# Kernel optimization log

Hardware: AMD Instinct MI355X
Metric: run time of the kernel (lower is better)

Reference implementation:

```python
import jax, jax.numpy as jnp
import numpy as np
from jax import lax

EPS = 1e-5  # flax BatchNorm default epsilon

def _conv(x, k, b):
    y = lax.conv_general_dilated(x, k, (1, 1), 'SAME', dimension_numbers=('NHWC', 'HWIO', 'NHWC'))
    return y + b

def _bn(x, s, o, m, v):
    # BatchNorm with use_running_average=True (eval mode)
    return (x - m) * (s / jnp.sqrt(v + EPS)) + o

def _pool(x):
    return lax.reduce_window(x, -jnp.inf, lax.max, (1, 2, 2, 1), (1, 2, 2, 1), 'SAME')

def _lstm_last(x_seq, Wi, Wh, b):
    # x_seq: [T,B,D]; Wi: [L,D,4H]; Wh: [L,H,4H]; b: [L,4H].
    # Faithful to original bug: every layer consumes the SAME raw input x_seq
    # (layers are not stacked); only the last layer's hidden states are used.
    B = x_seq.shape[1]
    H = Wh.shape[1]
    def run_layer(Wi_l, Wh_l, b_l):
        def step(carry, xt):
            h, c = carry
            z = xt @ Wi_l + h @ Wh_l + b_l  # [B,4H]
            i, f, g, o = jnp.split(z, 4, axis=-1)
            c2 = jax.nn.sigmoid(f) * c + jax.nn.sigmoid(i) * jnp.tanh(g)
            h2 = jax.nn.sigmoid(o) * jnp.tanh(c2)
            return (h2, c2), h2
        init = (jnp.zeros((B, H), x_seq.dtype), jnp.zeros((B, H), x_seq.dtype))
        _, hs = lax.scan(step, init, x_seq)
        return hs  # [T,B,H]
    hs_all = jax.vmap(run_layer)(Wi, Wh, b)  # [L,T,B,H]
    return hs_all[-1]


def setup_inputs():
    key = jax.random.key(0)
    ks = iter(jax.random.split(key, 64))
    def nrm(shape, scale=0.05):
        return jax.random.normal(next(ks), shape, jnp.float32) * scale
    d = {}
    d['x'] = jax.random.normal(next(ks), (64, 32, 256, 1), jnp.float32)
    cin = [1, 64, 128, 256, 256]
    cout = [64, 128, 256, 256, 512]
    for i in range(5):
        d[f'k{i+1}'] = nrm((3, 3, cin[i], cout[i]))
        d[f'b{i+1}'] = nrm((cout[i],))
        d[f's{i+1}'] = 1.0 + nrm((cout[i],), 0.1)
        d[f'o{i+1}'] = nrm((cout[i],), 0.1)
        d[f'm{i+1}'] = jnp.zeros((cout[i],), jnp.float32)
        d[f'v{i+1}'] = jnp.ones((cout[i],), jnp.float32)
    L, D, H = 2, 2048, 512
    for pre in ('fw', 'bw'):
        d[f'{pre}_Wi'] = nrm((L, D, 4 * H), 0.02)
        d[f'{pre}_Wh'] = nrm((L, H, 4 * H), 0.02)
        d[f'{pre}_b'] = nrm((L, 4 * H), 0.02)
    d['fc_W'] = nrm((2 * H, 80), 0.02)
    d['fc_b'] = nrm((80,), 0.02)
    return d


def reference(x, k1, b1, k2, b2, k3, b3, k4, b4, k5, b5,
              s1, o1, m1, v1, s2, o2, m2, v2, s3, o3, m3, v3,
              s4, o4, m4, v4, s5, o5, m5, v5,
              fw_Wi, fw_Wh, fw_b, bw_Wi, bw_Wh, bw_b, fc_W, fc_b):
    # CNN stem (eval mode: dropout is identity, BN uses running stats)
    x = _pool(_bn(jax.nn.relu(_conv(x, k1, b1)), s1, o1, m1, v1))
    x = _pool(_bn(jax.nn.relu(_conv(x, k2, b2)), s2, o2, m2, v2))
    x = _pool(_bn(jax.nn.relu(_conv(x, k3, b3)), s3, o3, m3, v3))
    x = _bn(jax.nn.relu(_conv(x, k4, b4)), s4, o4, m4, v4)
    x = _bn(jax.nn.relu(_conv(x, k5, b5)), s5, o5, m5, v5)
    b, h, w, c = x.shape
    x = x.reshape(b, w, h * c)        # faithful raw reshape (no transpose), as in original
    x_seq = jnp.swapaxes(x, 0, 1)     # [T,B,D]
    fw = _lstm_last(x_seq, fw_Wi, fw_Wh, fw_b)          # [T,B,H]
    bw = _lstm_last(x_seq[::-1], bw_Wi, bw_Wh, bw_b)    # [T,B,H]; NOT re-flipped (matches original)
    out = jnp.swapaxes(jnp.concatenate([fw, bw], axis=-1), 0, 1)  # [B,T,2H]
    logits = out @ fc_W + fc_b
    return jax.nn.log_softmax(logits, axis=-1)
```

## Files before the change

### kernel.cpp

```cpp
#include <hip/hip_runtime.h>
#include <hip/hip_bf16.h>
#include <math.h>

#define EPSBN 1e-5f

using short8 = __attribute__((ext_vector_type(8))) short;
using f32x4  = __attribute__((ext_vector_type(4))) float;
using us4    = __attribute__((ext_vector_type(4))) unsigned short;

#define MFMA16(a, b, c) __builtin_amdgcn_mfma_f32_16x16x32_bf16(a, b, c, 0, 0, 0)

__device__ __forceinline__ float bf2f(unsigned short u) {
  unsigned int v = ((unsigned int)u) << 16;
  float f;
  __builtin_memcpy(&f, &v, 4);
  return f;
}
__device__ __forceinline__ unsigned short f2bf(float f) {
  __hip_bfloat16 h = __float2bfloat16(f);
  unsigned short u;
  __builtin_memcpy(&u, &h, 2);
  return u;
}
__device__ __forceinline__ float fast_sigmoid(float z) {
  return __builtin_amdgcn_rcpf(1.f + __expf(-z));
}
__device__ __forceinline__ float fast_tanh(float z) {
  float x2 = fminf(fmaxf(2.f * z, -30.f), 30.f);
  float e = __expf(x2);
  return (e - 1.f) * __builtin_amdgcn_rcpf(e + 1.f);
}
__device__ __forceinline__ void stage16(const unsigned short* g, unsigned short* l) {
  __builtin_amdgcn_global_load_lds(
      (const __attribute__((address_space(1))) void*)g,
      (__attribute__((address_space(3))) void*)l, 16, 0, 0);
}

__global__ __launch_bounds__(256) void conv1_pool(
    const float* __restrict__ in, const float* __restrict__ w,
    const float* __restrict__ bias, const float* __restrict__ sc,
    const float* __restrict__ of, const float* __restrict__ mn,
    const float* __restrict__ vr, unsigned short* __restrict__ out) {
  __shared__ float lds[4][258];
  __shared__ unsigned short obuf[128 * 64];
  const int blk = blockIdx.x;
  const int b = blk >> 4, y0 = blk & 15;
  const int tid = threadIdx.x;
  for (int i = tid; i < 4 * 258; i += 256) {
    int row = i / 258, c = i - row * 258;
    int iy = 2 * y0 - 1 + row, xx = c - 1;
    float v = 0.f;
    if ((unsigned)iy < 32u && (unsigned)xx < 256u)
      v = in[((b << 5) + iy) * 256 + xx];
    lds[row][c] = v;
  }
  __syncthreads();
  const int co = tid & 63, xg = tid >> 6;
  float w9[9];
  #pragma unroll
  for (int t = 0; t < 9; ++t) w9[t] = w[t * 64 + co];
  const float scale = sc[co] * rsqrtf(vr[co] + EPSBN);
  const float shift = of[co] - mn[co] * scale;
  const float bs = bias[co];
  for (int px = 0; px < 32; ++px) {
    const int xp = xg * 32 + px;
    float m = -1e30f;
    #pragma unroll
    for (int dy = 0; dy < 2; ++dy) {
      #pragma unroll
      for (int dx = 0; dx < 2; ++dx) {
        const int x = 2 * xp + dx;
        float acc = bs;
        #pragma unroll
        for (int r = 0; r < 3; ++r)
          #pragma unroll
          for (int cc = 0; cc < 3; ++cc)
            acc = fmaf(lds[dy + r][x + cc], w9[r * 3 + cc], acc);
        float v = fmaxf(acc, 0.f) * scale + shift;
        m = fmaxf(m, v);
      }
    }
    obuf[xp * 64 + co] = f2bf(m);
  }
  __syncthreads();
  unsigned short* orow = out + (((long)(b * 18 + y0 + 1) * 130 + 1) << 6);
  for (int i = tid; i < 1024; i += 256)
    *(short8*)(orow + i * 8) = *(const short8*)(obuf + i * 8);
}

template<int C, int H2, int W2>
__global__ __launch_bounds__(256) void maxpool_pad_vec(
    const unsigned short* __restrict__ in, unsigned short* __restrict__ out) {
  constexpr int W2P = W2 + 2, H2P = H2 + 2, C8 = C / 8;
  const long total = (long)64 * H2P * W2P * C8;
  long i = (long)blockIdx.x * 256 + threadIdx.x;
  if (i >= total) return;
  const int c8 = (int)(i % C8);
  long r = i / C8;
  const int xp = (int)(r % W2P); r /= W2P;
  const int yp = (int)(r % H2P);
  const int b = (int)(r / H2P);
  short8 res = {};
  if (yp >= 1 && yp <= H2 && xp >= 1 && xp <= W2) {
    const long rs = (long)(2 * W2) * C;
    const unsigned short* p0 =
        in + (((long)b * (2 * H2) + (yp - 1) * 2) * (2 * W2) + (xp - 1) * 2) * C + c8 * 8;
    short8 v00 = *(const short8*)(p0);
    short8 v01 = *(const short8*)(p0 + C);
    short8 v10 = *(const short8*)(p0 + rs);
    short8 v11 = *(const short8*)(p0 + rs + C);
    #pragma unroll
    for (int e = 0; e < 8; ++e) {
      float f0 = bf2f((unsigned short)v00[e]), f1 = bf2f((unsigned short)v01[e]);
      float f2 = bf2f((unsigned short)v10[e]), f3 = bf2f((unsigned short)v11[e]);
      float mx = fmaxf(fmaxf(f0, f1), fmaxf(f2, f3));
      unsigned short uu;
      if (mx == f0) uu = (unsigned short)v00[e];
      else if (mx == f1) uu = (unsigned short)v01[e];
      else if (mx == f2) uu = (unsigned short)v10[e];
      else uu = (unsigned short)v11[e];
      res[e] = (short)uu;
    }
  }
  *(short8*)(out + (((long)b * H2P + yp) * W2P + xp) * C + c8 * 8) = res;
}

struct TAll {
  const float* src[9];
  unsigned short* dst[9];
  int K[9];
  int N[9];
};
__global__ __launch_bounds__(256) void transpose_multi(TAll P) {
  const int z = blockIdx.z;
  const int K = P.K[z], N = P.N[z];
  const int k0 = blockIdx.x * 32, n0 = blockIdx.y * 32;
  if (k0 >= K || n0 >= N) return;
  __shared__ float T[32][33];
  const float* in = P.src[z];
  unsigned short* out = P.dst[z];
  const int tid = threadIdx.x;
  const int r = tid >> 3, c4 = (tid & 7) * 4;
  if (n0 + 32 <= N) {
    float4 v = *(const float4*)(in + (long)(k0 + r) * N + n0 + c4);
    T[r][c4 + 0] = v.x; T[r][c4 + 1] = v.y; T[r][c4 + 2] = v.z; T[r][c4 + 3] = v.w;
  } else {
    #pragma unroll
    for (int i = 0; i < 4; ++i) {
      int col = n0 + c4 + i;
      T[r][c4 + i] = (col < N) ? in[(long)(k0 + r) * N + col] : 0.f;
    }
  }
  __syncthreads();
  if (n0 + r < N) {
    us4 o;
    #pragma unroll
    for (int i = 0; i < 4; ++i) o[i] = f2bf(T[c4 + i][r]);
    *(us4*)(out + (long)(n0 + r) * K + k0 + c4) = o;
  }
}

__global__ __launch_bounds__(256) void zero_multi(
    float* p0, long n0, float* p1, long n1, float* p2, long n2, float* p3, long n3) {
  const long i0 = (long)blockIdx.x * 256 + threadIdx.x;
  const long st = (long)gridDim.x * 256;
  for (long j = i0; j < n0; j += st) p0[j] = 0.f;
  for (long j = i0; j < n1; j += st) p1[j] = 0.f;
  for (long j = i0; j < n2; j += st) p2[j] = 0.f;
  for (long j = i0; j < n3; j += st) p3[j] = 0.f;
}

template<int CIN, int COUT, int H, int W, int OUTPAD, int NBM, int NBN>
__global__ __launch_bounds__(256) void conv_mfma128(
    const unsigned short* __restrict__ act, const unsigned short* __restrict__ wT,
    const float* __restrict__ bias, const float* __restrict__ sc,
    const float* __restrict__ of, const float* __restrict__ mn,
    const float* __restrict__ vr, unsigned short* __restrict__ out) {
  constexpr int K9 = 9 * CIN;
  constexpr int HW = H * W;
  constexpr int WP = W + 2;
  constexpr int NK = K9 / 32;
  constexpr int NWG = NBM * NBN;
  constexpr int CSH = (CIN == 64) ? 1 : (CIN == 128) ? 2 : 3;
  constexpr int CMSK = (1 << CSH) - 1;
  __shared__ unsigned short As[2][4096];
  __shared__ unsigned short Bs[2][4096];
  const int tid = threadIdx.x;
  const int lane = tid & 63, wave = tid >> 6;
  const int wzw = blockIdx.x;
  const int logical = (wzw & 7) * (NWG >> 3) + (wzw >> 3);
  const int m0 = (logical % NBM) * 128, n0 = (logical / NBM) * 128;
  const int r0 = tid >> 2, seg = tid & 3;
  const int segp = (seg ^ (r0 & 3)) << 3;
  long pa0, pa1;
  {
    const int m = m0 + r0;
    const int b = m / HW, rem = m % HW;
    const int y = rem / W, x = rem % W;
    pa0 = (((long)b * (H + 2) + y) * WP + x) * CIN + segp;
  }
  {
    const int m = m0 + r0 + 64;
    const int b = m / HW, rem = m % HW;
    const int y = rem / W, x = rem % W;
    pa1 = (((long)b * (H + 2) + y) * WP + x) * CIN + segp;
  }
  const long pb0 = (long)(n0 + r0) * K9 + segp;
  const long pb1 = (long)(n0 + r0 + 64) * K9 + segp;
  const int swz = ((lane >> 4) ^ (lane & 3)) << 3;
  const int arow0 = (wave >> 1) * 64 + (lane & 15);
  const int brow0 = (wave & 1) * 64 + (lane & 15);
  f32x4 acc[4][4] = {};

  auto stage_tile = [&](int ks, int buf) {
    const int tap = ks >> CSH;
    const int cib = (ks & CMSK) << 5;
    const int ty = (tap * 86) >> 8;
    const int tx = tap - ty * 3;
    const long ka = (long)(ty * WP + tx) * CIN + cib;
    const long kb = (long)ks << 5;
    unsigned short* aw = &As[buf][wave * 512];
    unsigned short* bw = &Bs[buf][wave * 512];
    stage16(act + pa0 + ka, aw);
    stage16(act + pa1 + ka, aw + 2048);
    stage16(wT + pb0 + kb, bw);
    stage16(wT + pb1 + kb, bw + 2048);
  };

  stage_tile(0, 0);
  #pragma unroll 1
  for (int ks = 0; ks < NK; ++ks) {
    const int buf = ks & 1;
    if (ks + 1 < NK) {
      stage_tile(ks + 1, buf ^ 1);
      asm volatile("s_waitcnt vmcnt(4)" ::: "memory");
    } else {
      asm volatile("s_waitcnt vmcnt(0)" ::: "memory");
    }
    __builtin_amdgcn_s_barrier();
    __builtin_amdgcn_sched_barrier(0);
    short8 a[4], b[4];
    #pragma unroll
    for (int i = 0; i < 4; ++i)
      a[i] = *(const short8*)(&As[buf][(arow0 + i * 16) * 32 + swz]);
    #pragma unroll
    for (int j = 0; j < 4; ++j)
      b[j] = *(const short8*)(&Bs[buf][(brow0 + j * 16) * 32 + swz]);
    #pragma unroll
    for (int i = 0; i < 4; ++i)
      #pragma unroll
      for (int j = 0; j < 4; ++j)
        acc[i][j] = MFMA16(a[i], b[j], acc[i][j]);
    __builtin_amdgcn_s_barrier();
    __builtin_amdgcn_sched_barrier(0);
  }

  float scl[4], shf[4], bsv[4];
  #pragma unroll
  for (int j = 0; j < 4; ++j) {
    const int col = n0 + (wave & 1) * 64 + j * 16 + (lane & 15);
    scl[j] = sc[col] * rsqrtf(vr[col] + EPSBN);
    shf[j] = of[col] - mn[col] * scl[j];
    bsv[j] = bias[col];
  }
  #pragma unroll
  for (int i = 0; i < 4; ++i) {
    #pragma unroll
    for (int rr = 0; rr < 4; ++rr) {
      const int m = m0 + (wave >> 1) * 64 + i * 16 + (lane >> 4) * 4 + rr;
      const int b = m / HW, rem = m % HW;
      const int y = rem / W, x = rem % W;
      long obase;
      if (OUTPAD) obase = (((long)b * (H + 2) + y + 1) * WP + x + 1) * COUT;
      else        obase = (((long)b * H + y) * W + x) * COUT;
      const int colb = n0 + (wave & 1) * 64 + (lane & 15);
      #pragma unroll
      for (int j = 0; j < 4; ++j) {
        const float v = fmaxf(acc[i][j][rr] + bsv[j], 0.f) * scl[j] + shf[j];
        out[obase + colb + j * 16] = f2bf(v);
      }
    }
  }
}

__global__ __launch_bounds__(256) void gemm_xw2(
    const unsigned short* __restrict__ src,
    const unsigned short* __restrict__ WiTF, const unsigned short* __restrict__ WiTB,
    const float* __restrict__ bF, const float* __restrict__ bB,
    float* __restrict__ xwFp, float* __restrict__ xwBp) {
  __shared__ unsigned short As[2][4096];
  __shared__ unsigned short Bs[2][4096];
  const int rev = blockIdx.z;
  const unsigned short* WiT = rev ? WiTB : WiTF;
  const float* bvec = rev ? bB : bF;
  float* xw = rev ? xwBp : xwFp;
  const int tid = threadIdx.x;
  const int lane = tid & 63, wave = tid >> 6;
  const int wzw = blockIdx.x;
  const int logical = (wzw & 7) * 32 + (wzw >> 3);
  const int m0 = (logical & 15) * 128, n0 = (logical >> 4) * 128;
  const int r0 = tid >> 2, seg = tid & 3;
  const int segp = (seg ^ (r0 & 3)) << 3;
  long pa0, pa1;
  {
    const int r = m0 + r0;
    const int t = r >> 6, bb = r & 63;
    const int tt = rev ? 31 - t : t;
    pa0 = (long)bb * 65536 + (long)tt * 2048 + segp;
  }
  {
    const int r = m0 + r0 + 64;
    const int t = r >> 6, bb = r & 63;
    const int tt = rev ? 31 - t : t;
    pa1 = (long)bb * 65536 + (long)tt * 2048 + segp;
  }
  const long pb0 = (long)(n0 + r0) * 2048 + segp;
  const long pb1 = (long)(n0 + r0 + 64) * 2048 + segp;
  const int swz = ((lane >> 4) ^ (lane & 3)) << 3;
  const int arow0 = (wave >> 1) * 64 + (lane & 15);
  const int brow0 = (wave & 1) * 64 + (lane & 15);
  f32x4 acc[4][4] = {};

  auto stage_tile = [&](int ks, int buf) {
    const long k0 = (long)ks << 5;
    unsigned short* aw = &As[buf][wave * 512];
    unsigned short* bw = &Bs[buf][wave * 512];
    stage16(src + pa0 + k0, aw);
    stage16(src + pa1 + k0, aw + 2048);
    stage16(WiT + pb0 + k0, bw);
    stage16(WiT + pb1 + k0, bw + 2048);
  };

  stage_tile(0, 0);
  #pragma unroll 1
  for (int ks = 0; ks < 64; ++ks) {
    const int buf = ks & 1;
    if (ks + 1 < 64) {
      stage_tile(ks + 1, buf ^ 1);
      asm volatile("s_waitcnt vmcnt(4)" ::: "memory");
    } else {
      asm volatile("s_waitcnt vmcnt(0)" ::: "memory");
    }
    __builtin_amdgcn_s_barrier();
    __builtin_amdgcn_sched_barrier(0);
    short8 a[4], b[4];
    #pragma unroll
    for (int i = 0; i < 4; ++i)
      a[i] = *(const short8*)(&As[buf][(arow0 + i * 16) * 32 + swz]);
    #pragma unroll
    for (int j = 0; j < 4; ++j)
      b[j] = *(const short8*)(&Bs[buf][(brow0 + j * 16) * 32 + swz]);
    #pragma unroll
    for (int i = 0; i < 4; ++i)
      #pragma unroll
      for (int j = 0; j < 4; ++j)
        acc[i][j] = MFMA16(a[i], b[j], acc[i][j]);
    __builtin_amdgcn_s_barrier();
    __builtin_amdgcn_sched_barrier(0);
  }

  float bsv[4];
  #pragma unroll
  for (int j = 0; j < 4; ++j)
    bsv[j] = bvec[n0 + (wave & 1) * 64 + j * 16 + (lane & 15)];
  #pragma unroll
  for (int i = 0; i < 4; ++i) {
    #pragma unroll
    for (int rr = 0; rr < 4; ++rr) {
      const int row = m0 + (wave >> 1) * 64 + i * 16 + (lane >> 4) * 4 + rr;
      const int colb = n0 + (wave & 1) * 64 + (lane & 15);
      #pragma unroll
      for (int j = 0; j < 4; ++j)
        xw[(long)row * 2048 + colb + j * 16] = acc[i][j][rr] + bsv[j];
    }
  }
}

__global__ __launch_bounds__(256) void lstm_persist(
    const unsigned short* __restrict__ WhTF, const unsigned short* __restrict__ WhTB,
    const float* __restrict__ xwF, const float* __restrict__ xwB,
    unsigned short* __restrict__ hsF, unsigned short* __restrict__ hsB,
    int* __restrict__ bar) {
  __shared__ unsigned short Whs[64 * 512];
  __shared__ unsigned short Hs[64 * 512];
  __shared__ float Zs[4 * 64 * 16];
  const int bid = blockIdx.x;
  const int dir = bid >> 5;
  const int nb = bid & 31;
  const int u0 = nb * 16;
  const unsigned short* WhT = dir ? WhTB : WhTF;
  const float* xw = dir ? xwB : xwF;
  unsigned short* hs = dir ? hsB : hsF;
  int* flagbase = bar + dir * 32 * 16;
  int* myflag = flagbase + nb * 16;
  const int tid = threadIdx.x;
  const int lane = tid & 63, wave = tid >> 6;
  const int lr = lane & 15, lk = lane >> 4;
  const int mp = wave >> 1, gp = wave & 1;

  #pragma unroll
  for (int i = 0; i < 16; ++i) {
    const int G = i * 256 + tid;
    const int row = G >> 6, g8 = G & 63;
    const int g = row >> 4, u = row & 15;
    short8 v = *(const short8*)(WhT + ((long)(g * 512 + u0 + u) << 9) + g8 * 8);
    *(short8*)(Whs + row * 512 + ((g8 ^ (row & 7)) << 3)) = v;
  }

  const int prow = tid >> 2;
  const int pu4 = (tid & 3) * 4;
  float c4[4] = {0.f, 0.f, 0.f, 0.f};
  float4 xq[4];
  #pragma unroll
  for (int g = 0; g < 4; ++g)
    xq[g] = *(const float4*)(xw + (long)prow * 2048 + g * 512 + u0 + pu4);

  for (int t = 0; t < 32; ++t) {
    const unsigned short* hsrc = hs + (long)t * 32768;
    #pragma unroll
    for (int i = 0; i < 16; ++i) {
      const int G = i * 256 + tid;
      const int row = G >> 6, g8 = G & 63;
      short8 v = *(const short8*)(hsrc + G * 8);
      *(short8*)(Hs + row * 512 + ((g8 ^ (row & 7)) << 3)) = v;
    }
    __syncthreads();

    f32x4 acc[2][2] = {};
    #pragma unroll
    for (int kk = 0; kk < 16; ++kk) {
      const int sw = ((lk + kk * 4) ^ (lr & 7)) << 3;
      short8 a0 = *(const short8*)(Hs + (mp * 32 + lr) * 512 + sw);
      short8 a1 = *(const short8*)(Hs + (mp * 32 + 16 + lr) * 512 + sw);
      short8 b0 = *(const short8*)(Whs + (gp * 32 + lr) * 512 + sw);
      short8 b1 = *(const short8*)(Whs + (gp * 32 + 16 + lr) * 512 + sw);
      acc[0][0] = MFMA16(a0, b0, acc[0][0]);
      acc[0][1] = MFMA16(a0, b1, acc[0][1]);
      acc[1][0] = MFMA16(a1, b0, acc[1][0]);
      acc[1][1] = MFMA16(a1, b1, acc[1][1]);
    }

    #pragma unroll
    for (int im = 0; im < 2; ++im) {
      const int rowb = (mp * 2 + im) * 16 + lk * 4;
      #pragma unroll
      for (int ig = 0; ig < 2; ++ig) {
        const int g = gp * 2 + ig;
        #pragma unroll
        for (int r = 0; r < 4; ++r)
          Zs[g * 1024 + (rowb + r) * 16 + lr] = acc[im][ig][r];
      }
    }
    __syncthreads();

    {
      float4 zi = *(const float4*)(Zs + tid * 4);
      float4 zf = *(const float4*)(Zs + 1024 + tid * 4);
      float4 zg = *(const float4*)(Zs + 2048 + tid * 4);
      float4 zo = *(const float4*)(Zs + 3072 + tid * 4);
      const float* pzi = (const float*)&zi;
      const float* pzf = (const float*)&zf;
      const float* pzg = (const float*)&zg;
      const float* pzo = (const float*)&zo;
      us4 hv;
      #pragma unroll
      for (int r = 0; r < 4; ++r) {
        float ii = fast_sigmoid(pzi[r] + ((const float*)&xq[0])[r]);
        float ff = fast_sigmoid(pzf[r] + ((const float*)&xq[1])[r]);
        float gg = fast_tanh(pzg[r] + ((const float*)&xq[2])[r]);
        float oo = fast_sigmoid(pzo[r] + ((const float*)&xq[3])[r]);
        c4[r] = ff * c4[r] + ii * gg;
        hv[r] = f2bf(oo * fast_tanh(c4[r]));
      }
      *(us4*)(hs + (long)(t + 1) * 32768 + prow * 512 + u0 + pu4) = hv;
    }

    if (t < 31) {
      float4 xqn[4];
      #pragma unroll
      for (int g = 0; g < 4; ++g)
        xqn[g] = *(const float4*)(xw + (long)((t + 1) * 64 + prow) * 2048 + g * 512 + u0 + pu4);
      __syncthreads();
      if (tid < 64) {
        if (tid == 0)
          __hip_atomic_store(myflag, t + 1, __ATOMIC_RELEASE, __HIP_MEMORY_SCOPE_AGENT);
        int v;
        do {
          v = __hip_atomic_load(flagbase + (tid & 31) * 16,
                                __ATOMIC_RELAXED, __HIP_MEMORY_SCOPE_AGENT);
        } while (__any(v < t + 1));
      }
      __syncthreads();
      __builtin_amdgcn_fence(__ATOMIC_ACQUIRE, "agent");
      #pragma unroll
      for (int g = 0; g < 4; ++g) xq[g] = xqn[g];
    }
  }
}

__global__ __launch_bounds__(256) void fc_mfma_ls(
    const unsigned short* __restrict__ hsF, const unsigned short* __restrict__ hsB,
    const unsigned short* __restrict__ WT, const float* __restrict__ bias,
    float* __restrict__ out) {
  __shared__ unsigned short As_[128 * 32];
  __shared__ unsigned short Bs_[80 * 32];
  __shared__ float zbuf[128][81];
  __shared__ float rmax[128];
  __shared__ float rlse[128];
  const int tid = threadIdx.x;
  const int lane = tid & 63, wave = tid >> 6;
  const int m0 = blockIdx.x * 128;
  const int r0 = tid >> 2, seg = tid & 3;
  const int segp = (seg ^ (r0 & 3)) << 3;
  const int swz = ((lane >> 4) ^ (lane & 3)) << 3;
  f32x4 acc[2][5] = {};

  int bA0, tA0, bA1, tA1;
  { int r = m0 + r0;      bA0 = r >> 5; tA0 = r & 31; }
  { int r = m0 + r0 + 64; bA1 = r >> 5; tA1 = r & 31; }

  #pragma unroll 1
  for (int k0 = 0; k0 < 1024; k0 += 32) {
    const unsigned short* src = (k0 < 512) ? hsF : hsB;
    const int koff = k0 & 511;
    stage16(src + (long)(tA0 + 1) * 32768 + bA0 * 512 + koff + segp, As_ + wave * 512);
    stage16(src + (long)(tA1 + 1) * 32768 + bA1 * 512 + koff + segp, As_ + wave * 512 + 2048);
    {
      int G = tid;
      #pragma unroll
      for (int it = 0; it < 2; ++it, G += 256) {
        int rn = G >> 2, sg = G & 3;
        if (rn < 80) {
          short8 v = *(const short8*)(WT + (long)rn * 1024 + k0 + sg * 8);
          *(short8*)(Bs_ + rn * 32 + ((sg ^ (rn & 3)) << 3)) = v;
        }
      }
    }
    __syncthreads();
    short8 a[2], bfrag[5];
    #pragma unroll
    for (int i = 0; i < 2; ++i)
      a[i] = *(const short8*)(As_ + (wave * 32 + i * 16 + (lane & 15)) * 32 + swz);
    #pragma unroll
    for (int j = 0; j < 5; ++j)
      bfrag[j] = *(const short8*)(Bs_ + (j * 16 + (lane & 15)) * 32 + swz);
    #pragma unroll
    for (int i = 0; i < 2; ++i)
      #pragma unroll
      for (int j = 0; j < 5; ++j)
        acc[i][j] = MFMA16(a[i], bfrag[j], acc[i][j]);
    __syncthreads();
  }

  float bsv[5];
  #pragma unroll
  for (int j = 0; j < 5; ++j) bsv[j] = bias[j * 16 + (lane & 15)];
  #pragma unroll
  for (int i = 0; i < 2; ++i)
    #pragma unroll
    for (int j = 0; j < 5; ++j)
      #pragma unroll
      for (int rr = 0; rr < 4; ++rr)
        zbuf[wave * 32 + i * 16 + (lane >> 4) * 4 + rr][j * 16 + (lane & 15)] =
            acc[i][j][rr] + bsv[j];
  __syncthreads();

  if (tid < 128) {
    float mx = -1e30f;
    for (int j = 0; j < 80; ++j) mx = fmaxf(mx, zbuf[tid][j]);
    float s = 0.f;
    for (int j = 0; j < 80; ++j) s += __expf(zbuf[tid][j] - mx);
    rmax[tid] = mx;
    rlse[tid] = logf(s);
  }
  __syncthreads();

  for (int idx = tid; idx < 128 * 80; idx += 256) {
    const int row = idx / 80, j = idx - row * 80;
    out[(long)m0 * 80 + idx] = zbuf[row][j] - rmax[row] - rlse[row];
  }
}

extern "C" void kernel_launch(void* const* d_in, const int* in_sizes, int n_in,
                              void* d_out, int out_size, void* d_ws, size_t ws_size,
                              hipStream_t stream) {
  const float* x  = (const float*)d_in[0];
  const float* k1 = (const float*)d_in[1];  const float* b1 = (const float*)d_in[2];
  const float* s1 = (const float*)d_in[3];  const float* o1 = (const float*)d_in[4];
  const float* m1 = (const float*)d_in[5];  const float* v1 = (const float*)d_in[6];
  const float* k2 = (const float*)d_in[7];  const float* b2 = (const float*)d_in[8];
  const float* s2 = (const float*)d_in[9];  const float* o2 = (const float*)d_in[10];
  const float* m2 = (const float*)d_in[11]; const float* v2 = (const float*)d_in[12];
  const float* k3 = (const float*)d_in[13]; const float* b3 = (const float*)d_in[14];
  const float* s3 = (const float*)d_in[15]; const float* o3 = (const float*)d_in[16];
  const float* m3 = (const float*)d_in[17]; const float* v3 = (const float*)d_in[18];
  const float* k4 = (const float*)d_in[19]; const float* b4 = (const float*)d_in[20];
  const float* s4 = (const float*)d_in[21]; const float* o4 = (const float*)d_in[22];
  const float* m4 = (const float*)d_in[23]; const float* v4 = (const float*)d_in[24];
  const float* k5 = (const float*)d_in[25]; const float* b5 = (const float*)d_in[26];
  const float* s5 = (const float*)d_in[27]; const float* o5 = (const float*)d_in[28];
  const float* m5 = (const float*)d_in[29]; const float* v5 = (const float*)d_in[30];
  const float* fwWi = (const float*)d_in[31];
  const float* fwWh = (const float*)d_in[32];
  const float* fwb  = (const float*)d_in[33];
  const float* bwWi = (const float*)d_in[34];
  const float* bwWh = (const float*)d_in[35];
  const float* bwb  = (const float*)d_in[36];
  const float* fcW  = (const float*)d_in[37];
  const float* fcb  = (const float*)d_in[38];

  char* wsb = (char*)d_ws;
  unsigned short* REG_A = (unsigned short*)(wsb);
  unsigned short* REG_P = (unsigned short*)(wsb + 33554432);
  unsigned short* C4    = (unsigned short*)(wsb + 52723712);
  unsigned short* wT2   = (unsigned short*)(wsb + 59408384);
  unsigned short* wT3   = (unsigned short*)(wsb + 59555840);
  unsigned short* wT4   = (unsigned short*)(wsb + 60145664);
  unsigned short* wT5   = (unsigned short*)(wsb + 61325312);
  unsigned short* WiTF  = (unsigned short*)(wsb + 63684608);
  unsigned short* WiTB  = (unsigned short*)(wsb + 72073216);
  unsigned short* WhTF  = (unsigned short*)(wsb + 80461824);
  unsigned short* WhTB  = (unsigned short*)(wsb + 82558976);
  unsigned short* WTfc  = (unsigned short*)(wsb + 84656128);
  float* xwF = (float*)(wsb + 84819968);
  float* xwB = (float*)(wsb + 101597184);
  int*   bar = (int*)(wsb + 118374400);
  unsigned short* hsF = (unsigned short*)(wsb + 118378496);
  unsigned short* hsB = (unsigned short*)(wsb + 120541184);

  zero_multi<<<2048, 256, 0, stream>>>(
      (float*)(wsb + 118374400), 17408,
      (float*)(wsb + 120541184), 16384,
      (float*)(wsb + 52723712), 1671168,
      (float*)(wsb + 33554432), 4792320);

  TAll tp;
  tp.src[0] = k2; tp.dst[0] = wT2; tp.K[0] = 576;  tp.N[0] = 128;
  tp.src[1] = k3; tp.dst[1] = wT3; tp.K[1] = 1152; tp.N[1] = 256;
  tp.src[2] = k4; tp.dst[2] = wT4; tp.K[2] = 2304; tp.N[2] = 256;
  tp.src[3] = k5; tp.dst[3] = wT5; tp.K[3] = 2304; tp.N[3] = 512;
  tp.src[4] = fwWi + 4194304; tp.dst[4] = WiTF; tp.K[4] = 2048; tp.N[4] = 2048;
  tp.src[5] = bwWi + 4194304; tp.dst[5] = WiTB; tp.K[5] = 2048; tp.N[5] = 2048;
  tp.src[6] = fwWh + 1048576; tp.dst[6] = WhTF; tp.K[6] = 512;  tp.N[6] = 2048;
  tp.src[7] = bwWh + 1048576; tp.dst[7] = WhTB; tp.K[7] = 512;  tp.N[7] = 2048;
  tp.src[8] = fcW; tp.dst[8] = WTfc; tp.K[8] = 1024; tp.N[8] = 80;
  transpose_multi<<<dim3(72, 64, 9), 256, 0, stream>>>(tp);

  conv1_pool<<<1024, 256, 0, stream>>>(x, k1, b1, s1, o1, m1, v1, REG_P);

  conv_mfma128<64, 128, 16, 128, 0, 1024, 1><<<1024, 256, 0, stream>>>(
      REG_P, wT2, b2, s2, o2, m2, v2, REG_A);
  maxpool_pad_vec<128, 8, 64><<<2640, 256, 0, stream>>>(REG_A, REG_P);

  conv_mfma128<128, 256, 8, 64, 0, 256, 2><<<512, 256, 0, stream>>>(
      REG_P, wT3, b3, s3, o3, m3, v3, REG_A);
  maxpool_pad_vec<256, 4, 32><<<1632, 256, 0, stream>>>(REG_A, REG_P);

  conv_mfma128<256, 256, 4, 32, 1, 64, 2><<<128, 256, 0, stream>>>(
      REG_P, wT4, b4, s4, o4, m4, v4, C4);

  conv_mfma128<256, 512, 4, 32, 0, 64, 4><<<256, 256, 0, stream>>>(
      C4, wT5, b5, s5, o5, m5, v5, REG_A);

  gemm_xw2<<<dim3(256, 1, 2), 256, 0, stream>>>(
      REG_A, WiTF, WiTB, fwb + 2048, bwb + 2048, xwF, xwB);

  lstm_persist<<<64, 256, 0, stream>>>(WhTF, WhTB, xwF, xwB, hsF, hsB, bar);

  fc_mfma_ls<<<16, 256, 0, stream>>>(hsF, hsB, WTfc, fcb, (float*)d_out);
}
```

Before: 487.2 us.

## Fuse 2x2 max-pool into conv2/conv3 MFMA epilogues and zero only halos

Adds a conv_pool_mfma kernel whose 128-row M tile covers two adjacent output rows of 64 pixels. After the BN epilogue it pools 2x2 through LDS and writes the padded pooled tensor directly, which removes the two standalone maxpool kernels and their full-resolution activation round trips. The full-buffer zeroing pass becomes a halo-only zeroing kernel, and the workspace is relaid into separate padded buffers. The LSTM spin-wait now uses acquire loads in place of relaxed loads plus a separate fence. This changes the tile-to-pixel mapping, and the halo-only zeroing depends on every interior element being written.

```diff
diff --git a/kernel.cpp b/kernel.cpp
--- a/kernel.cpp
+++ b/kernel.cpp
@@ -86,43 +86,6 @@
   unsigned short* orow = out + (((long)(b * 18 + y0 + 1) * 130 + 1) << 6);
   for (int i = tid; i < 1024; i += 256)
     *(short8*)(orow + i * 8) = *(const short8*)(obuf + i * 8);
-}
-
-template<int C, int H2, int W2>
-__global__ __launch_bounds__(256) void maxpool_pad_vec(
-    const unsigned short* __restrict__ in, unsigned short* __restrict__ out) {
-  constexpr int W2P = W2 + 2, H2P = H2 + 2, C8 = C / 8;
-  const long total = (long)64 * H2P * W2P * C8;
-  long i = (long)blockIdx.x * 256 + threadIdx.x;
-  if (i >= total) return;
-  const int c8 = (int)(i % C8);
-  long r = i / C8;
-  const int xp = (int)(r % W2P); r /= W2P;
-  const int yp = (int)(r % H2P);
-  const int b = (int)(r / H2P);
-  short8 res = {};
-  if (yp >= 1 && yp <= H2 && xp >= 1 && xp <= W2) {
-    const long rs = (long)(2 * W2) * C;
-    const unsigned short* p0 =
-        in + (((long)b * (2 * H2) + (yp - 1) * 2) * (2 * W2) + (xp - 1) * 2) * C + c8 * 8;
-    short8 v00 = *(const short8*)(p0);
-    short8 v01 = *(const short8*)(p0 + C);
-    short8 v10 = *(const short8*)(p0 + rs);
-    short8 v11 = *(const short8*)(p0 + rs + C);
-    #pragma unroll
-    for (int e = 0; e < 8; ++e) {
-      float f0 = bf2f((unsigned short)v00[e]), f1 = bf2f((unsigned short)v01[e]);
-      float f2 = bf2f((unsigned short)v10[e]), f3 = bf2f((unsigned short)v11[e]);
-      float mx = fmaxf(fmaxf(f0, f1), fmaxf(f2, f3));
-      unsigned short uu;
-      if (mx == f0) uu = (unsigned short)v00[e];
-      else if (mx == f1) uu = (unsigned short)v01[e];
-      else if (mx == f2) uu = (unsigned short)v10[e];
-      else uu = (unsigned short)v11[e];
-      res[e] = (short)uu;
-    }
-  }
-  *(short8*)(out + (((long)b * H2P + yp) * W2P + xp) * C + c8 * 8) = res;
 }
 
 struct TAll {
@@ -160,14 +123,182 @@
   }
 }
 
-__global__ __launch_bounds__(256) void zero_multi(
-    float* p0, long n0, float* p1, long n1, float* p2, long n2, float* p3, long n3) {
+struct ZHP {
+  unsigned short* p[4];
+  int HP[4], WP[4], C[4];
+};
+__global__ __launch_bounds__(256) void zero_halos(
+    ZHP Z, float* __restrict__ f0, long n0, float* __restrict__ f1, long n1) {
   const long i0 = (long)blockIdx.x * 256 + threadIdx.x;
   const long st = (long)gridDim.x * 256;
-  for (long j = i0; j < n0; j += st) p0[j] = 0.f;
-  for (long j = i0; j < n1; j += st) p1[j] = 0.f;
-  for (long j = i0; j < n2; j += st) p2[j] = 0.f;
-  for (long j = i0; j < n3; j += st) p3[j] = 0.f;
+  short8 z = {};
+  #pragma unroll
+  for (int t = 0; t < 4; ++t) {
+    unsigned short* p = Z.p[t];
+    const int HP = Z.HP[t], WP = Z.WP[t], C = Z.C[t];
+    const long rc = (long)WP * C / 8;
+    const long tot_r = 64L * 2 * rc;
+    for (long j = i0; j < tot_r; j += st) {
+      long b = j / (2 * rc), r = j % (2 * rc);
+      int y = (r >= rc) ? (HP - 1) : 0;
+      long c = (r >= rc) ? r - rc : r;
+      *(short8*)(p + (((long)b * HP + y) * WP) * C + c * 8) = z;
+    }
+    const long cc = C / 8;
+    const long grp = (long)(HP - 2) * 2 * cc;
+    const long tot_c = 64L * grp;
+    for (long j = i0; j < tot_c; j += st) {
+      long b = j / grp, r = j % grp;
+      int y = 1 + (int)(r / (2 * cc));
+      long r2 = r % (2 * cc);
+      int x = (r2 >= cc) ? (WP - 1) : 0;
+      long c = (r2 >= cc) ? r2 - cc : r2;
+      *(short8*)(p + (((long)b * HP + y) * WP + x) * C + c * 8) = z;
+    }
+  }
+  for (long j = i0; j < n0; j += st) f0[j] = 0.f;
+  for (long j = i0; j < n1; j += st) f1[j] = 0.f;
+}
+
+template<int CIN, int COUT, int H, int W, int NBM, int NBN>
+__global__ __launch_bounds__(256) void conv_pool_mfma(
+    const unsigned short* __restrict__ act, const unsigned short* __restrict__ wT,
+    const float* __restrict__ bias, const float* __restrict__ sc,
+    const float* __restrict__ of, const float* __restrict__ mn,
+    const float* __restrict__ vr, unsigned short* __restrict__ out) {
+  constexpr int K9 = 9 * CIN;
+  constexpr int WP = W + 2;
+  constexpr int NK = K9 / 32;
+  constexpr int NWG = NBM * NBN;
+  constexpr int TX = W / 64;
+  constexpr int H2 = H / 2;
+  constexpr int HPO = H2 + 2, WPO = W / 2 + 2;
+  constexpr int CSH = (CIN == 64) ? 1 : (CIN == 128) ? 2 : 3;
+  constexpr int CMSK = (1 << CSH) - 1;
+  __shared__ unsigned short SM[16384];
+  unsigned short* As0 = SM;
+  unsigned short* Bs0 = SM + 8192;
+  const int tid = threadIdx.x;
+  const int lane = tid & 63, wave = tid >> 6;
+  const int wzw = blockIdx.x;
+  const int logical = (wzw & 7) * (NWG >> 3) + (wzw >> 3);
+  const int mt = logical % NBM;
+  const int n0 = (logical / NBM) * 128;
+  const int tx = mt % TX;
+  const int t2 = mt / TX;
+  const int yh = t2 % H2;
+  const int bb = t2 / H2;
+  const int r0 = tid >> 2, seg = tid & 3;
+  const int segp = (seg ^ (r0 & 3)) << 3;
+  const long pa0 = (((long)bb * (H + 2) + 2 * yh) * WP + tx * 64 + r0) * CIN + segp;
+  const long pa1 = (((long)bb * (H + 2) + 2 * yh + 1) * WP + tx * 64 + r0) * CIN + segp;
+  const long pb0 = (long)(n0 + r0) * K9 + segp;
+  const long pb1 = (long)(n0 + r0 + 64) * K9 + segp;
+  const int swz = ((lane >> 4) ^ (lane & 3)) << 3;
+  const int arow0 = (wave >> 1) * 64 + (lane & 15);
+  const int brow0 = (wave & 1) * 64 + (lane & 15);
+  f32x4 acc[4][4] = {};
+
+  auto stage_tile = [&](int ks, int buf) {
+    const int tap = ks >> CSH;
+    const int cib = (ks & CMSK) << 5;
+    const int ty = (tap * 86) >> 8;
+    const int txp = tap - ty * 3;
+    const long ka = (long)(ty * WP + txp) * CIN + cib;
+    const long kb = (long)ks << 5;
+    unsigned short* aw = As0 + buf * 4096 + wave * 512;
+    unsigned short* bw = Bs0 + buf * 4096 + wave * 512;
+    stage16(act + pa0 + ka, aw);
+    stage16(act + pa1 + ka, aw + 2048);
+    stage16(wT + pb0 + kb, bw);
+    stage16(wT + pb1 + kb, bw + 2048);
+  };
+
+  stage_tile(0, 0);
+  #pragma unroll 1
+  for (int ks = 0; ks < NK; ++ks) {
+    const int buf = ks & 1;
+    if (ks + 1 < NK) {
+      stage_tile(ks + 1, buf ^ 1);
+      asm volatile("s_waitcnt vmcnt(4)" ::: "memory");
+    } else {
+      asm volatile("s_waitcnt vmcnt(0)" ::: "memory");
+    }
+    __builtin_amdgcn_s_barrier();
+    __builtin_amdgcn_sched_barrier(0);
+    short8 a[4], b[4];
+    #pragma unroll
+    for (int i = 0; i < 4; ++i)
+      a[i] = *(const short8*)(As0 + buf * 4096 + (arow0 + i * 16) * 32 + swz);
+    #pragma unroll
+    for (int j = 0; j < 4; ++j)
+      b[j] = *(const short8*)(Bs0 + buf * 4096 + (brow0 + j * 16) * 32 + swz);
+    #pragma unroll
+    for (int i = 0; i < 4; ++i)
+      #pragma unroll
+      for (int j = 0; j < 4; ++j)
+        acc[i][j] = MFMA16(a[i], b[j], acc[i][j]);
+    __builtin_amdgcn_s_barrier();
+    __builtin_amdgcn_sched_barrier(0);
+  }
+
+  float scl[4], shf[4], bsv[4];
+  #pragma unroll
+  for (int j = 0; j < 4; ++j) {
+    const int col = n0 + (wave & 1) * 64 + j * 16 + (lane & 15);
+    scl[j] = sc[col] * rsqrtf(vr[col] + EPSBN);
+    shf[j] = of[col] - mn[col] * scl[j];
+    bsv[j] = bias[col];
+  }
+  #pragma unroll
+  for (int i = 0; i < 4; ++i) {
+    #pragma unroll
+    for (int rr = 0; rr < 4; ++rr) {
+      const int mrow = (wave >> 1) * 64 + i * 16 + (lane >> 4) * 4 + rr;
+      const int collb = (wave & 1) * 64 + (lane & 15);
+      #pragma unroll
+      for (int j = 0; j < 4; ++j) {
+        const float v = fmaxf(acc[i][j][rr] + bsv[j], 0.f) * scl[j] + shf[j];
+        SM[mrow * 128 + collb + j * 16] = f2bf(v);
+      }
+    }
+  }
+  __syncthreads();
+
+  const int q = tid >> 3, cg = (tid & 7) * 16;
+  short8 p00a = *(const short8*)(SM + (2 * q) * 128 + cg);
+  short8 p00b = *(const short8*)(SM + (2 * q) * 128 + cg + 8);
+  short8 p01a = *(const short8*)(SM + (2 * q + 1) * 128 + cg);
+  short8 p01b = *(const short8*)(SM + (2 * q + 1) * 128 + cg + 8);
+  short8 p10a = *(const short8*)(SM + (64 + 2 * q) * 128 + cg);
+  short8 p10b = *(const short8*)(SM + (64 + 2 * q) * 128 + cg + 8);
+  short8 p11a = *(const short8*)(SM + (64 + 2 * q + 1) * 128 + cg);
+  short8 p11b = *(const short8*)(SM + (64 + 2 * q + 1) * 128 + cg + 8);
+  short8 oa, ob;
+  #pragma unroll
+  for (int e = 0; e < 8; ++e) {
+    float f0 = bf2f((unsigned short)p00a[e]), f1 = bf2f((unsigned short)p01a[e]);
+    float f2 = bf2f((unsigned short)p10a[e]), f3 = bf2f((unsigned short)p11a[e]);
+    float mx = fmaxf(fmaxf(f0, f1), fmaxf(f2, f3));
+    unsigned short uu;
+    if (mx == f0) uu = (unsigned short)p00a[e];
+    else if (mx == f1) uu = (unsigned short)p01a[e];
+    else if (mx == f2) uu = (unsigned short)p10a[e];
+    else uu = (unsigned short)p11a[e];
+    oa[e] = (short)uu;
+    float g0 = bf2f((unsigned short)p00b[e]), g1 = bf2f((unsigned short)p01b[e]);
+    float g2 = bf2f((unsigned short)p10b[e]), g3 = bf2f((unsigned short)p11b[e]);
+    float my = fmaxf(fmaxf(g0, g1), fmaxf(g2, g3));
+    if (my == g0) uu = (unsigned short)p00b[e];
+    else if (my == g1) uu = (unsigned short)p01b[e];
+    else if (my == g2) uu = (unsigned short)p10b[e];
+    else uu = (unsigned short)p11b[e];
+    ob[e] = (short)uu;
+  }
+  unsigned short* op = out +
+      (((long)bb * HPO + 1 + yh) * WPO + 1 + tx * 32 + q) * COUT + n0 + cg;
+  *(short8*)op = oa;
+  *(short8*)(op + 8) = ob;
 }
 
 template<int CIN, int COUT, int H, int W, int OUTPAD, int NBM, int NBN>
@@ -487,11 +618,10 @@
         int v;
         do {
           v = __hip_atomic_load(flagbase + (tid & 31) * 16,
-                                __ATOMIC_RELAXED, __HIP_MEMORY_SCOPE_AGENT);
+                                __ATOMIC_ACQUIRE, __HIP_MEMORY_SCOPE_AGENT);
         } while (__any(v < t + 1));
       }
       __syncthreads();
-      __builtin_amdgcn_fence(__ATOMIC_ACQUIRE, "agent");
       #pragma unroll
       for (int g = 0; g < 4; ++g) xq[g] = xqn[g];
     }
@@ -611,28 +741,32 @@
 
   char* wsb = (char*)d_ws;
   unsigned short* REG_A = (unsigned short*)(wsb);
-  unsigned short* REG_P = (unsigned short*)(wsb + 33554432);
-  unsigned short* C4    = (unsigned short*)(wsb + 52723712);
-  unsigned short* wT2   = (unsigned short*)(wsb + 59408384);
-  unsigned short* wT3   = (unsigned short*)(wsb + 59555840);
-  unsigned short* wT4   = (unsigned short*)(wsb + 60145664);
-  unsigned short* wT5   = (unsigned short*)(wsb + 61325312);
-  unsigned short* WiTF  = (unsigned short*)(wsb + 63684608);
-  unsigned short* WiTB  = (unsigned short*)(wsb + 72073216);
-  unsigned short* WhTF  = (unsigned short*)(wsb + 80461824);
-  unsigned short* WhTB  = (unsigned short*)(wsb + 82558976);
-  unsigned short* WTfc  = (unsigned short*)(wsb + 84656128);
-  float* xwF = (float*)(wsb + 84819968);
-  float* xwB = (float*)(wsb + 101597184);
-  int*   bar = (int*)(wsb + 118374400);
-  unsigned short* hsF = (unsigned short*)(wsb + 118378496);
-  unsigned short* hsB = (unsigned short*)(wsb + 120541184);
-
-  zero_multi<<<2048, 256, 0, stream>>>(
-      (float*)(wsb + 118374400), 17408,
-      (float*)(wsb + 120541184), 16384,
-      (float*)(wsb + 52723712), 1671168,
-      (float*)(wsb + 33554432), 4792320);
+  unsigned short* P1    = (unsigned short*)(wsb + 8388608);
+  unsigned short* P2    = (unsigned short*)(wsb + 27557888);
+  unsigned short* P3    = (unsigned short*)(wsb + 38371328);
+  unsigned short* C4    = (unsigned short*)(wsb + 45056000);
+  unsigned short* wT2   = (unsigned short*)(wsb + 51740672);
+  unsigned short* wT3   = (unsigned short*)(wsb + 51888128);
+  unsigned short* wT4   = (unsigned short*)(wsb + 52477952);
+  unsigned short* wT5   = (unsigned short*)(wsb + 53657600);
+  unsigned short* WiTF  = (unsigned short*)(wsb + 56016896);
+  unsigned short* WiTB  = (unsigned short*)(wsb + 64405504);
+  unsigned short* WhTF  = (unsigned short*)(wsb + 72794112);
+  unsigned short* WhTB  = (unsigned short*)(wsb + 74891264);
+  unsigned short* WTfc  = (unsigned short*)(wsb + 76988416);
+  float* xwF = (float*)(wsb + 77152256);
+  float* xwB = (float*)(wsb + 93929472);
+  int*   bar = (int*)(wsb + 110706688);
+  unsigned short* hsF = (unsigned short*)(wsb + 110710784);
+  unsigned short* hsB = (unsigned short*)(wsb + 112873472);
+
+  ZHP zh;
+  zh.p[0] = P1; zh.HP[0] = 18; zh.WP[0] = 130; zh.C[0] = 64;
+  zh.p[1] = P2; zh.HP[1] = 10; zh.WP[1] = 66;  zh.C[1] = 128;
+  zh.p[2] = P3; zh.HP[2] = 6;  zh.WP[2] = 34;  zh.C[2] = 256;
+  zh.p[3] = C4; zh.HP[3] = 6;  zh.WP[3] = 34;  zh.C[3] = 256;
+  zero_halos<<<512, 256, 0, stream>>>(
+      zh, (float*)(wsb + 110706688), 17408, (float*)(wsb + 112873472), 16384);
 
   TAll tp;
   tp.src[0] = k2; tp.dst[0] = wT2; tp.K[0] = 576;  tp.N[0] = 128;
@@ -646,18 +780,16 @@
   tp.src[8] = fcW; tp.dst[8] = WTfc; tp.K[8] = 1024; tp.N[8] = 80;
   transpose_multi<<<dim3(72, 64, 9), 256, 0, stream>>>(tp);
 
-  conv1_pool<<<1024, 256, 0, stream>>>(x, k1, b1, s1, o1, m1, v1, REG_P);
-
-  conv_mfma128<64, 128, 16, 128, 0, 1024, 1><<<1024, 256, 0, stream>>>(
-      REG_P, wT2, b2, s2, o2, m2, v2, REG_A);
-  maxpool_pad_vec<128, 8, 64><<<2640, 256, 0, stream>>>(REG_A, REG_P);
-
-  conv_mfma128<128, 256, 8, 64, 0, 256, 2><<<512, 256, 0, stream>>>(
-      REG_P, wT3, b3, s3, o3, m3, v3, REG_A);
-  maxpool_pad_vec<256, 4, 32><<<1632, 256, 0, stream>>>(REG_A, REG_P);
+  conv1_pool<<<1024, 256, 0, stream>>>(x, k1, b1, s1, o1, m1, v1, P1);
+
+  conv_pool_mfma<64, 128, 16, 128, 1024, 1><<<1024, 256, 0, stream>>>(
+      P1, wT2, b2, s2, o2, m2, v2, P2);
+
+  conv_pool_mfma<128, 256, 8, 64, 256, 2><<<512, 256, 0, stream>>>(
+      P2, wT3, b3, s3, o3, m3, v3, P3);
 
   conv_mfma128<256, 256, 4, 32, 1, 64, 2><<<128, 256, 0, stream>>>(
-      REG_P, wT4, b4, s4, o4, m4, v4, C4);
+      P3, wT4, b4, s4, o4, m4, v4, C4);
 
   conv_mfma128<256, 512, 4, 32, 0, 64, 4><<<256, 256, 0, stream>>>(
       C4, wT5, b5, s5, o5, m5, v5, REG_A);
```

New measurement: 444.5 us. 1.1x faster.
